# Kernel tuning notes

Hardware: AMD Instinct MI355X
Metric: run time of the kernel (lower is better)

Reference implementation:

```python
import jax, jax.numpy as jnp
import numpy as np

TAU = 0.05
EPS = 1e-12


def _l2_normalize(x):
    # F.normalize(p=2): x / max(||x||, eps)
    n = jnp.sqrt(jnp.sum(x * x, axis=-1, keepdims=True))
    return x / jnp.maximum(n, EPS)


def _masked_lse(sim, mask):
    # logsumexp over axis -1 restricted to mask; rows with empty mask are
    # masked out downstream (has_pos), so we guard the log to stay finite.
    neg_inf = jnp.finfo(sim.dtype).min
    mx = jnp.max(jnp.where(mask, sim, neg_inf), axis=-1)
    mx_safe = jnp.where(mx > neg_inf / 2, mx, 0.0)
    s = jnp.sum(jnp.where(mask, jnp.exp(sim - mx_safe[:, None]), 0.0), axis=-1)
    return mx_safe + jnp.log(jnp.where(s > 0, s, 1.0))


def setup_inputs() -> dict:
    key = jax.random.key(0)
    k1, k2, k3, k4 = jax.random.split(key, 4)
    B, S, D = 64, 128, 256
    return {
        "logits": jax.random.normal(k1, (B, S, D), dtype=jnp.float32),
        "labels": jax.random.normal(k2, (B, S, D), dtype=jnp.float32),
        "pad_mask": jax.random.randint(k3, (B, S), 0, 2, dtype=jnp.int32),
        "ad_idxs": jax.random.randint(k4, (B, S), 0, 500, dtype=jnp.int32),
    }


def reference(logits, labels, pad_mask, ad_idxs):
    B, S, D = logits.shape
    q = _l2_normalize(logits.reshape(B * S, D))
    k = _l2_normalize(labels.reshape(B * S, D))
    valid = pad_mask.reshape(B * S).astype(bool)
    ad = ad_idxs.reshape(B * S)

    sim = jnp.einsum("nd,md->nm", q, k) / TAU          # [N, N]
    pair_valid = valid[None, :] & valid[:, None]
    pos_mask = (ad[None, :] == ad[:, None]) & pair_valid

    pos_lse = _masked_lse(sim, pos_mask)
    all_lse = _masked_lse(sim, pair_valid)
    has_pos = jnp.any(pos_mask, axis=-1)

    loss_per_row = -(pos_lse - all_lse)
    # mean over rows with at least one positive (== loss_per_row[has_pos].mean())
    cnt = jnp.sum(has_pos.astype(sim.dtype))
    loss = jnp.sum(jnp.where(has_pos, loss_per_row, 0.0)) / jnp.maximum(cnt, 1.0)
    return loss
```

## Files before the change

### kernel.cpp

```cpp
#include <hip/hip_runtime.h>
#include <hip/hip_bf16.h>
#include <hip/hip_fp8.h>
#include <math.h>

typedef float f32x4 __attribute__((ext_vector_type(4)));
typedef int   i32x4 __attribute__((ext_vector_type(4)));
typedef int   v8i   __attribute__((ext_vector_type(8)));

constexpr int Nn = 8192;
constexpr int Dd = 256;
constexpr float LOG2E     = 1.4426950408889634f;
constexpr float SIM_SCALE = 20.0f * LOG2E;
constexpr float SIM_BIAS  = -20.0f * LOG2E;
constexpr int   SCALE1    = 0x7F7F7F7F;

typedef __attribute__((address_space(1))) const unsigned int gu32;
typedef __attribute__((address_space(3))) unsigned int lu32;
__device__ __forceinline__ void gload16(const unsigned char* g, unsigned char* l) {
  __builtin_amdgcn_global_load_lds((gu32*)(uintptr_t)g, (lu32*)(uintptr_t)l, 16, 0, 0);
}

#define VMCNT4() asm volatile("s_waitcnt vmcnt(4)" ::: "memory")
#define VMCNT0() asm volatile("s_waitcnt vmcnt(0)" ::: "memory")
#define LGKM0()  asm volatile("s_waitcnt lgkmcnt(0)" ::: "memory")
#define SCHEDB() __builtin_amdgcn_sched_barrier(0)
#define BAR()    __builtin_amdgcn_s_barrier()

__global__ __launch_bounds__(256) void prep_kernel(const float* __restrict__ logits,
                                                   const float* __restrict__ labels,
                                                   const int* __restrict__ pad,
                                                   unsigned char* __restrict__ qb,
                                                   unsigned char* __restrict__ kb,
                                                   float* __restrict__ cbias,
                                                   float* __restrict__ g_all,
                                                   float* __restrict__ g_pos) {
  const int j = blockIdx.x * 256 + threadIdx.x;
  if (j < Nn) {
    cbias[j] = pad[j] ? SIM_BIAS : -1e30f;
    g_all[j] = 0.0f;
    g_pos[j] = 0.0f;
  }

  const int gw   = (blockIdx.x * 256 + threadIdx.x) >> 6;
  const int lane = threadIdx.x & 63;
  const float* src;
  unsigned char* dst;
  int row;
  if (gw < Nn) { src = logits; dst = qb; row = gw; }
  else         { src = labels; dst = kb; row = gw - Nn; }

  const float4 v = *reinterpret_cast<const float4*>(src + (size_t)row * Dd + lane * 4);
  float ss = v.x * v.x + v.y * v.y + v.z * v.z + v.w * v.w;
#pragma unroll
  for (int m = 32; m >= 1; m >>= 1) ss += __shfl_xor(ss, m);
  const float scale = 1.0f / fmaxf(sqrtf(ss), 1e-12f);

  const __hip_fp8_e4m3 e0(v.x * scale);
  const __hip_fp8_e4m3 e1(v.y * scale);
  const __hip_fp8_e4m3 e2(v.z * scale);
  const __hip_fp8_e4m3 e3(v.w * scale);
  const unsigned int packed = (unsigned int)e0.__x |
                              ((unsigned int)e1.__x << 8) |
                              ((unsigned int)e2.__x << 16) |
                              ((unsigned int)e3.__x << 24);
  reinterpret_cast<unsigned int*>(dst + (size_t)row * Dd)[lane] = packed;
}

__global__ __launch_bounds__(256, 2) void gemm_lse_kernel(const unsigned char* __restrict__ qb,
                                                          const unsigned char* __restrict__ kb,
                                                          const float* __restrict__ cbias,
                                                          const int* __restrict__ ad,
                                                          float* __restrict__ g_all,
                                                          float* __restrict__ g_pos) {
  __shared__ unsigned char smem[49152];

  const int tid  = threadIdx.x;
  const int lane = tid & 63;
  const int w    = tid >> 6;
  const int wrow  = (w >> 1) * 64;
  const int wcolL = (w & 1) * 64;
  const int lq   = lane & 15;
  const int qd   = lane >> 4;
  const int rowBase = blockIdx.x * 128;
  const int colBase = blockIdx.y * 1024;

  const int srl = lane >> 3;
  const int cg  = (lane & 7) ^ srl;
  const unsigned char* gA0 = qb + (size_t)(rowBase + w * 32 + srl) * Dd + cg * 16;
  const unsigned char* gB0 = kb + (size_t)(colBase + w * 32 + srl) * Dd + cg * 16;

#pragma unroll
  for (int kk = 0; kk < 2; ++kk)
#pragma unroll
    for (int i = 0; i < 4; ++i)
      gload16(gA0 + (size_t)i * 8 * Dd + kk * 128,
              &smem[kk * 16384 + (w * 32 + i * 8) * 128]);
#pragma unroll
  for (int i = 0; i < 4; ++i)
    gload16(gB0 + (size_t)i * 8 * Dd, &smem[32768 + (w * 32 + i * 8) * 128]);

  int rowAd[4][4];
#pragma unroll
  for (int mt = 0; mt < 4; ++mt)
#pragma unroll
    for (int r = 0; r < 4; ++r)
      rowAd[mt][r] = ad[rowBase + wrow + mt * 16 + qd * 4 + r];

  float apA[4][4], apP[4][4];
#pragma unroll
  for (int mt = 0; mt < 4; ++mt)
#pragma unroll
    for (int r = 0; r < 4; ++r) {
      apA[mt][r] = 0.f;
      apP[mt][r] = 0.f;
    }

  VMCNT4();
  BAR();

  const int sl = lq & 7;
  const int s0 = ((qd * 2) ^ sl) << 4;
  const int s1 = ((qd * 2 + 1) ^ sl) << 4;

  v8i afReg[2][4];
#pragma unroll
  for (int kk = 0; kk < 2; ++kk) {
    const unsigned char* Ah = &smem[kk * 16384];
#pragma unroll
    for (int mt = 0; mt < 4; ++mt) {
      const int rb = (wrow + mt * 16 + lq) * 128;
      i32x4* ph_ = reinterpret_cast<i32x4*>(&afReg[kk][mt]);
      ph_[0] = *reinterpret_cast<const i32x4*>(&Ah[rb + s0]);
      ph_[1] = *reinterpret_cast<const i32x4*>(&Ah[rb + s1]);
    }
  }

  __syncthreads();

  {
    unsigned char* dB = &smem[0 + (w * 32) * 128];
    const unsigned char* g = gB0 + 128;
#pragma unroll
    for (int i = 0; i < 4; ++i)
      gload16(g + (size_t)i * 8 * Dd, dB + i * 8 * 128);
  }

  const f32x4 CZ = (f32x4){0.f, 0.f, 0.f, 0.f};
  f32x4 c[4][4];
  float colB[4];
  int colAd[4];

  for (int ct = 0; ct < 8; ++ct) {
    const int sA = (2 * ct) % 3;
    const unsigned bas0 = (sA == 0) ? 32768u : ((sA == 1) ? 0u : 16384u);
    const unsigned bas1 = (sA == 2) ? 32768u : ((sA == 0) ? 0u : 16384u);
    const unsigned bas2 = (sA == 1) ? 32768u : ((sA == 2) ? 0u : 16384u);
    const unsigned bas3 = bas0;

    {
      VMCNT4();
      BAR();

#pragma unroll
      for (int nt = 0; nt < 4; ++nt) {
        const int col = colBase + ct * 128 + wcolL + nt * 16 + lq;
        colB[nt]  = cbias[col];
        colAd[nt] = ad[col];
      }

      if (ct < 7) {
        unsigned char* dB = &smem[bas2 + (w * 32) * 128];
        const unsigned char* g = gB0 + (size_t)((ct + 1) * 128) * Dd;
#pragma unroll
        for (int i = 0; i < 4; ++i)
          gload16(g + (size_t)i * 8 * Dd, dB + i * 8 * 128);
      }

      const unsigned char* Bh = &smem[bas0];
#pragma unroll
      for (int nt = 0; nt < 4; ++nt) {
        const int rb = (wcolL + nt * 16 + lq) * 128;
        v8i bf;
        i32x4* pb = reinterpret_cast<i32x4*>(&bf);
        pb[0] = *reinterpret_cast<const i32x4*>(&Bh[rb + s0]);
        pb[1] = *reinterpret_cast<const i32x4*>(&Bh[rb + s1]);
#pragma unroll
        for (int mt = 0; mt < 4; ++mt)
          c[mt][nt] = __builtin_amdgcn_mfma_scale_f32_16x16x128_f8f6f4(
              afReg[0][mt], bf, CZ, 0, 0, 0, SCALE1, 0, SCALE1);
      }
      LGKM0();
      SCHEDB();
    }

    {
      if (ct < 7) { VMCNT4(); } else { VMCNT0(); }
      BAR();

      if (ct < 7) {
        unsigned char* dB = &smem[bas3 + (w * 32) * 128];
        const unsigned char* g = gB0 + (size_t)((ct + 1) * 128) * Dd + 128;
#pragma unroll
        for (int i = 0; i < 4; ++i)
          gload16(g + (size_t)i * 8 * Dd, dB + i * 8 * 128);
      }

      const unsigned char* Bh = &smem[bas1];
#pragma unroll
      for (int nt = 0; nt < 4; ++nt) {
        const int rb = (wcolL + nt * 16 + lq) * 128;
        v8i bf;
        i32x4* pb = reinterpret_cast<i32x4*>(&bf);
        pb[0] = *reinterpret_cast<const i32x4*>(&Bh[rb + s0]);
        pb[1] = *reinterpret_cast<const i32x4*>(&Bh[rb + s1]);
#pragma unroll
        for (int mt = 0; mt < 4; ++mt)
          c[mt][nt] = __builtin_amdgcn_mfma_scale_f32_16x16x128_f8f6f4(
              afReg[1][mt], bf, c[mt][nt], 0, 0, 0, SCALE1, 0, SCALE1);
      }
      LGKM0();
      SCHEDB();

#pragma unroll
      for (int mt = 0; mt < 4; ++mt) {
#pragma unroll
        for (int r = 0; r < 4; ++r) {
          float a = 0.f, p = 0.f;
#pragma unroll
          for (int nt = 0; nt < 4; ++nt) {
            const float e = __builtin_amdgcn_exp2f(fmaf(c[mt][nt][r], SIM_SCALE, colB[nt]));
            a += e;
            p += (colAd[nt] == rowAd[mt][r]) ? e : 0.f;
          }
          apA[mt][r] += a;
          apP[mt][r] += p;
        }
      }
    }
  }

#pragma unroll
  for (int mt = 0; mt < 4; ++mt) {
#pragma unroll
    for (int r = 0; r < 4; ++r) {
      float a = apA[mt][r], p = apP[mt][r];
#pragma unroll
      for (int m = 1; m < 16; m <<= 1) {
        a += __shfl_xor(a, m);
        p += __shfl_xor(p, m);
      }
      if (lq == 0) {
        const int row = rowBase + wrow + mt * 16 + qd * 4 + r;
        atomicAdd(&g_all[row], a);
        atomicAdd(&g_pos[row], p);
      }
    }
  }
}

__global__ __launch_bounds__(1024) void reduce_kernel(const float* __restrict__ g_all,
                                                      const float* __restrict__ g_pos,
                                                      const int* __restrict__ pad,
                                                      float* __restrict__ out) {
  __shared__ float sS[16], sC[16];
  const int t = threadIdx.x;
  float s = 0.f, c = 0.f;
  const float4* ga4 = (const float4*)g_all;
  const float4* gp4 = (const float4*)g_pos;
  const int4*   pd4 = (const int4*)pad;
  for (int i = t; i < Nn / 4; i += 1024) {
    const float4 ga = ga4[i];
    const float4 gp = gp4[i];
    const int4   pd = pd4[i];
    if (pd.x) { s += __logf(ga.x) - __logf(gp.x); c += 1.f; }
    if (pd.y) { s += __logf(ga.y) - __logf(gp.y); c += 1.f; }
    if (pd.z) { s += __logf(ga.z) - __logf(gp.z); c += 1.f; }
    if (pd.w) { s += __logf(ga.w) - __logf(gp.w); c += 1.f; }
  }
#pragma unroll
  for (int m = 32; m >= 1; m >>= 1) {
    s += __shfl_xor(s, m);
    c += __shfl_xor(c, m);
  }
  if ((t & 63) == 0) { sS[t >> 6] = s; sC[t >> 6] = c; }
  __syncthreads();
  if (t == 0) {
    float S = 0.f, C = 0.f;
#pragma unroll
    for (int i = 0; i < 16; ++i) { S += sS[i]; C += sC[i]; }
    out[0] = S / fmaxf(C, 1.0f);
  }
}

extern "C" void kernel_launch(void* const* d_in, const int* in_sizes, int n_in,
                              void* d_out, int out_size, void* d_ws, size_t ws_size,
                              hipStream_t stream) {
  const float* logits = (const float*)d_in[0];
  const float* labels = (const float*)d_in[1];
  const int*   pad    = (const int*)d_in[2];
  const int*   ad     = (const int*)d_in[3];

  char* ws = (char*)d_ws;
  unsigned char* qb = (unsigned char*)(ws);
  unsigned char* kb = (unsigned char*)(ws + 2097152);
  float*  cb   = (float*)(ws + 4194304);
  float*  gAll = (float*)(ws + 4227072);
  float*  gPos = (float*)(ws + 4259840);
  float*  out  = (float*)d_out;

  prep_kernel<<<4096, 256, 0, stream>>>(logits, labels, pad, qb, kb, cb, gAll, gPos);
  gemm_lse_kernel<<<dim3(64, 8), 256, 0, stream>>>(qb, kb, cb, ad, gAll, gPos);
  reduce_kernel<<<1, 1024, 0, stream>>>(gAll, gPos, pad, out);
}
```

Before: 100.1 us.

## Compute positive-pair sums from per-ad bucket lists instead of in GEMM epilogue

The GEMM epilogue no longer compares ad indices and accumulates positive-pair exponentials per tile. Instead, valid rows are bucketed by ad index into per-ad lists, and a new kernel computes each row's positive sum from dot products against only its bucket members. That kernel also folds in the final log-ratio reduction using a last-block-done atomic, replacing the separate reduce kernel. This lightens the epilogue's register and ALU load, but adds scattered fp8 gathers and a fixed bucket capacity that would silently drop positives if any ad id had more than 512 valid members.

```diff
diff --git a/kernel.cpp b/kernel.cpp
--- a/kernel.cpp
+++ b/kernel.cpp
@@ -13,6 +13,7 @@
 constexpr float SIM_SCALE = 20.0f * LOG2E;
 constexpr float SIM_BIAS  = -20.0f * LOG2E;
 constexpr int   SCALE1    = 0x7F7F7F7F;
+constexpr int   BCAP      = 512;
 
 typedef __attribute__((address_space(1))) const unsigned int gu32;
 typedef __attribute__((address_space(3))) unsigned int lu32;
@@ -25,6 +26,10 @@
 #define LGKM0()  asm volatile("s_waitcnt lgkmcnt(0)" ::: "memory")
 #define SCHEDB() __builtin_amdgcn_sched_barrier(0)
 #define BAR()    __builtin_amdgcn_s_barrier()
+
+__device__ __forceinline__ float fp8f(unsigned int b) {
+  __hip_fp8_e4m3 v; v.__x = (unsigned char)(b & 0xffu); return (float)v;
+}
 
 __global__ __launch_bounds__(256) void prep_kernel(const float* __restrict__ logits,
                                                    const float* __restrict__ labels,
@@ -33,13 +38,17 @@
                                                    unsigned char* __restrict__ kb,
                                                    float* __restrict__ cbias,
                                                    float* __restrict__ g_all,
-                                                   float* __restrict__ g_pos) {
+                                                   int* __restrict__ cnt,
+                                                   float* __restrict__ accS,
+                                                   float* __restrict__ accC,
+                                                   int* __restrict__ done) {
   const int j = blockIdx.x * 256 + threadIdx.x;
   if (j < Nn) {
     cbias[j] = pad[j] ? SIM_BIAS : -1e30f;
     g_all[j] = 0.0f;
-    g_pos[j] = 0.0f;
-  }
+  }
+  if (j < BCAP) cnt[j] = 0;
+  if (j == 0) { *accS = 0.f; *accC = 0.f; *done = 0; }
 
   const int gw   = (blockIdx.x * 256 + threadIdx.x) >> 6;
   const int lane = threadIdx.x & 63;
@@ -70,11 +79,23 @@
                                                           const unsigned char* __restrict__ kb,
                                                           const float* __restrict__ cbias,
                                                           const int* __restrict__ ad,
+                                                          const int* __restrict__ pad,
                                                           float* __restrict__ g_all,
-                                                          float* __restrict__ g_pos) {
+                                                          int* __restrict__ cnt,
+                                                          int* __restrict__ lists) {
   __shared__ unsigned char smem[49152];
 
   const int tid  = threadIdx.x;
+
+  if (blockIdx.y == 0) {
+    const int t = blockIdx.x * 256 + tid;
+    if (t < Nn && pad[t]) {
+      const int a = ad[t];
+      const int slot = atomicAdd(&cnt[a], 1);
+      if (slot < BCAP) lists[a * BCAP + slot] = t;
+    }
+  }
+
   const int lane = tid & 63;
   const int w    = tid >> 6;
   const int wrow  = (w >> 1) * 64;
@@ -99,21 +120,12 @@
   for (int i = 0; i < 4; ++i)
     gload16(gB0 + (size_t)i * 8 * Dd, &smem[32768 + (w * 32 + i * 8) * 128]);
 
-  int rowAd[4][4];
+  float apA[4][4];
 #pragma unroll
   for (int mt = 0; mt < 4; ++mt)
 #pragma unroll
     for (int r = 0; r < 4; ++r)
-      rowAd[mt][r] = ad[rowBase + wrow + mt * 16 + qd * 4 + r];
-
-  float apA[4][4], apP[4][4];
-#pragma unroll
-  for (int mt = 0; mt < 4; ++mt)
-#pragma unroll
-    for (int r = 0; r < 4; ++r) {
       apA[mt][r] = 0.f;
-      apP[mt][r] = 0.f;
-    }
 
   VMCNT4();
   BAR();
@@ -148,7 +160,6 @@
   const f32x4 CZ = (f32x4){0.f, 0.f, 0.f, 0.f};
   f32x4 c[4][4];
   float colB[4];
-  int colAd[4];
 
   for (int ct = 0; ct < 8; ++ct) {
     const int sA = (2 * ct) % 3;
@@ -162,11 +173,8 @@
       BAR();
 
 #pragma unroll
-      for (int nt = 0; nt < 4; ++nt) {
-        const int col = colBase + ct * 128 + wcolL + nt * 16 + lq;
-        colB[nt]  = cbias[col];
-        colAd[nt] = ad[col];
-      }
+      for (int nt = 0; nt < 4; ++nt)
+        colB[nt] = cbias[colBase + ct * 128 + wcolL + nt * 16 + lq];
 
       if (ct < 7) {
         unsigned char* dB = &smem[bas2 + (w * 32) * 128];
@@ -225,15 +233,11 @@
       for (int mt = 0; mt < 4; ++mt) {
 #pragma unroll
         for (int r = 0; r < 4; ++r) {
-          float a = 0.f, p = 0.f;
-#pragma unroll
-          for (int nt = 0; nt < 4; ++nt) {
-            const float e = __builtin_amdgcn_exp2f(fmaf(c[mt][nt][r], SIM_SCALE, colB[nt]));
-            a += e;
-            p += (colAd[nt] == rowAd[mt][r]) ? e : 0.f;
-          }
+          float a = 0.f;
+#pragma unroll
+          for (int nt = 0; nt < 4; ++nt)
+            a += __builtin_amdgcn_exp2f(fmaf(c[mt][nt][r], SIM_SCALE, colB[nt]));
           apA[mt][r] += a;
-          apP[mt][r] += p;
         }
       }
     }
@@ -243,52 +247,80 @@
   for (int mt = 0; mt < 4; ++mt) {
 #pragma unroll
     for (int r = 0; r < 4; ++r) {
-      float a = apA[mt][r], p = apP[mt][r];
-#pragma unroll
-      for (int m = 1; m < 16; m <<= 1) {
+      float a = apA[mt][r];
+#pragma unroll
+      for (int m = 1; m < 16; m <<= 1)
         a += __shfl_xor(a, m);
-        p += __shfl_xor(p, m);
-      }
       if (lq == 0) {
         const int row = rowBase + wrow + mt * 16 + qd * 4 + r;
         atomicAdd(&g_all[row], a);
-        atomicAdd(&g_pos[row], p);
-      }
-    }
-  }
-}
-
-__global__ __launch_bounds__(1024) void reduce_kernel(const float* __restrict__ g_all,
-                                                      const float* __restrict__ g_pos,
-                                                      const int* __restrict__ pad,
-                                                      float* __restrict__ out) {
-  __shared__ float sS[16], sC[16];
-  const int t = threadIdx.x;
-  float s = 0.f, c = 0.f;
-  const float4* ga4 = (const float4*)g_all;
-  const float4* gp4 = (const float4*)g_pos;
-  const int4*   pd4 = (const int4*)pad;
-  for (int i = t; i < Nn / 4; i += 1024) {
-    const float4 ga = ga4[i];
-    const float4 gp = gp4[i];
-    const int4   pd = pd4[i];
-    if (pd.x) { s += __logf(ga.x) - __logf(gp.x); c += 1.f; }
-    if (pd.y) { s += __logf(ga.y) - __logf(gp.y); c += 1.f; }
-    if (pd.z) { s += __logf(ga.z) - __logf(gp.z); c += 1.f; }
-    if (pd.w) { s += __logf(ga.w) - __logf(gp.w); c += 1.f; }
-  }
-#pragma unroll
-  for (int m = 32; m >= 1; m >>= 1) {
-    s += __shfl_xor(s, m);
-    c += __shfl_xor(c, m);
-  }
-  if ((t & 63) == 0) { sS[t >> 6] = s; sC[t >> 6] = c; }
+      }
+    }
+  }
+}
+
+__global__ __launch_bounds__(256) void pos_loss_kernel(const unsigned char* __restrict__ qb,
+                                                       const unsigned char* __restrict__ kb,
+                                                       const float* __restrict__ g_all,
+                                                       const int* __restrict__ pad,
+                                                       const int* __restrict__ ad,
+                                                       const int* __restrict__ cnt,
+                                                       const int* __restrict__ lists,
+                                                       float* __restrict__ accS,
+                                                       float* __restrict__ accC,
+                                                       int* __restrict__ done,
+                                                       float* __restrict__ out,
+                                                       int nblocks) {
+  const int tid  = threadIdx.x;
+  const int lane = tid & 63;
+  const int w    = tid >> 6;
+  const int row  = blockIdx.x * 4 + w;
+
+  float sTerm = 0.f, cTerm = 0.f;
+  if (pad[row]) {
+    const unsigned int qw =
+        reinterpret_cast<const unsigned int*>(qb + (size_t)row * Dd)[lane];
+    const float q0 = fp8f(qw), q1 = fp8f(qw >> 8),
+                q2 = fp8f(qw >> 16), q3 = fp8f(qw >> 24);
+    const int a = ad[row];
+    int m = cnt[a];
+    if (m > BCAP) m = BCAP;
+    const int* lst = lists + a * BCAP;
+
+    float p = 0.f;
+    unsigned int kw =
+        reinterpret_cast<const unsigned int*>(kb + (size_t)lst[0] * Dd)[lane];
+    for (int s = 0; s < m; ++s) {
+      const unsigned int kwc = kw;
+      if (s + 1 < m)
+        kw = reinterpret_cast<const unsigned int*>(kb + (size_t)lst[s + 1] * Dd)[lane];
+      float d = q0 * fp8f(kwc);
+      d = fmaf(q1, fp8f(kwc >> 8), d);
+      d = fmaf(q2, fp8f(kwc >> 16), d);
+      d = fmaf(q3, fp8f(kwc >> 24), d);
+#pragma unroll
+      for (int mm = 32; mm >= 1; mm >>= 1) d += __shfl_xor(d, mm);
+      p += __builtin_amdgcn_exp2f(fmaf(d, SIM_SCALE, SIM_BIAS));
+    }
+    if (lane == 0) {
+      sTerm = __logf(g_all[row]) - __logf(p);
+      cTerm = 1.f;
+    }
+  }
+
+  __shared__ float bS[4], bC[4];
+  if (lane == 0) { bS[w] = sTerm; bC[w] = cTerm; }
   __syncthreads();
-  if (t == 0) {
-    float S = 0.f, C = 0.f;
-#pragma unroll
-    for (int i = 0; i < 16; ++i) { S += sS[i]; C += sC[i]; }
-    out[0] = S / fmaxf(C, 1.0f);
+  if (tid == 0) {
+    atomicAdd(accS, (bS[0] + bS[1]) + (bS[2] + bS[3]));
+    atomicAdd(accC, (bC[0] + bC[1]) + (bC[2] + bC[3]));
+    __threadfence();
+    const int old = atomicAdd(done, 1);
+    if (old == nblocks - 1) {
+      const float S = atomicAdd(accS, 0.f);
+      const float C = atomicAdd(accC, 0.f);
+      out[0] = S / fmaxf(C, 1.f);
+    }
   }
 }
 
@@ -303,12 +335,19 @@
   char* ws = (char*)d_ws;
   unsigned char* qb = (unsigned char*)(ws);
   unsigned char* kb = (unsigned char*)(ws + 2097152);
-  float*  cb   = (float*)(ws + 4194304);
-  float*  gAll = (float*)(ws + 4227072);
-  float*  gPos = (float*)(ws + 4259840);
-  float*  out  = (float*)d_out;
-
-  prep_kernel<<<4096, 256, 0, stream>>>(logits, labels, pad, qb, kb, cb, gAll, gPos);
-  gemm_lse_kernel<<<dim3(64, 8), 256, 0, stream>>>(qb, kb, cb, ad, gAll, gPos);
-  reduce_kernel<<<1, 1024, 0, stream>>>(gAll, gPos, pad, out);
-}
+  float* cb    = (float*)(ws + 4194304);
+  float* gAll  = (float*)(ws + 4227072);
+  int*   cnt   = (int*)  (ws + 4259840);
+  float* accS  = (float*)(ws + 4261888);
+  float* accC  = (float*)(ws + 4261892);
+  int*   done  = (int*)  (ws + 4261896);
+  int*   lists = (int*)  (ws + 4325376);
+  float* out   = (float*)d_out;
+
+  prep_kernel<<<4096, 256, 0, stream>>>(logits, labels, pad, qb, kb, cb, gAll,
+                                        cnt, accS, accC, done);
+  gemm_lse_kernel<<<dim3(64, 8), 256, 0, stream>>>(qb, kb, cb, ad, pad, gAll,
+                                                   cnt, lists);
+  pos_loss_kernel<<<2048, 256, 0, stream>>>(qb, kb, gAll, pad, ad, cnt, lists,
+                                            accS, accC, done, out, 2048);
+}
```

Result: slower. 174.3 us (+74.1%).
